# Optimization experiments

Measured on AMD Instinct MI355X. Metric: run time of the kernel, lower is better.

Reference implementation:

```python
import jax, jax.numpy as jnp
import numpy as np

# Sizes: B graphs of N nodes each, K nearest neighbours, D=feat_dim=nhid, C=pos_dim
B, N, K, D, C = 4, 1024, 128, 32, 2
L = 3                     # number of EGNN conv layers
E_IN = 2 * D + 1          # edge MLP input: feats_i | feats_j | rel_dist (edge_dim=0, fourier=0)
E_H = 2 * E_IN            # edge MLP hidden


def _lin(key, fan_in, fan_out):
    kw, kb = jax.random.split(key)
    w = jax.random.normal(kw, (fan_in, fan_out), jnp.float32) / np.sqrt(fan_in)
    b = jax.random.normal(kb, (fan_out,), jnp.float32) * 0.01
    return w, b


def _stack(key, fan_in, fan_out):
    ws, bs = zip(*[_lin(k, fan_in, fan_out) for k in jax.random.split(key, L)])
    return jnp.stack(ws), jnp.stack(bs)


def setup_inputs() -> dict:
    key = jax.random.key(0)
    ks = jax.random.split(key, 10)
    feat_ = jax.random.normal(ks[0], (B * N, D), jnp.float32)
    coor_ = jax.random.normal(ks[1], (B * N, C), jnp.float32)
    batch = jnp.full((B,), N, dtype=jnp.int32)   # per-graph node counts (equal-size graphs)
    embed_w, embed_b = _lin(ks[2], D, D)         # embed: Linear(feat_dim, nhid)
    e1_w, e1_b = _stack(ks[3], E_IN, E_H)        # edge MLP
    e2_w, e2_b = _stack(ks[4], E_H, D)           # -> m_dim = nhid
    gate_w, gate_b = _stack(ks[5], D, 1)         # soft_edges gate
    c1_w, c1_b = _stack(ks[6], D, 4 * D)         # coors MLP
    c2_w, c2_b = _stack(ks[7], 4 * D, 1)
    n1_w, n1_b = _stack(ks[8], 2 * D, 2 * D)     # node MLP
    n2_w, n2_b = _stack(ks[9], 2 * D, D)
    coors_scale = jnp.full((L, 1), 1e-2, jnp.float32)  # CoorsNorm scale (init 1e-2)
    return dict(feat_=feat_, coor_=coor_, batch=batch, embed_w=embed_w, embed_b=embed_b,
                e1_w=e1_w, e1_b=e1_b, e2_w=e2_w, e2_b=e2_b, gate_w=gate_w, gate_b=gate_b,
                c1_w=c1_w, c1_b=c1_b, c2_w=c2_w, c2_b=c2_b, n1_w=n1_w, n1_b=n1_b,
                n2_w=n2_w, n2_b=n2_b, coors_scale=coors_scale)


def _lrelu(x):
    return jax.nn.leaky_relu(x, 0.1)


def _gather(x, idx):
    # x: [B, n, d], idx: [B, n, k] -> [B, n, k, d]
    return jax.vmap(lambda xb, ib: xb[ib])(x, idx)


def _egnn_layer(feats, coors, p):
    (e1_w, e1_b, e2_w, e2_b, gate_w, gate_b, c1_w, c1_b, c2_w, c2_b,
     n1_w, n1_b, n2_w, n2_b, scale) = p
    # pairwise squared distances; k smallest (self included, valid_radius=inf)
    diff = coors[:, :, None, :] - coors[:, None, :, :]      # [B,n,n,C]
    dist = jnp.sum(diff * diff, axis=-1)                    # [B,n,n]
    neg_d, idx = jax.lax.top_k(-dist, K)                    # k nearest
    rel_dist = -neg_d[..., None]                            # [B,n,K,1]
    rel_coors = coors[:, :, None, :] - _gather(coors, idx)  # [B,n,K,C]
    feats_j = _gather(feats, idx)                           # [B,n,K,D]
    feats_i = jnp.broadcast_to(feats[:, :, None, :], feats_j.shape)
    edge_in = jnp.concatenate([feats_i, feats_j, rel_dist], axis=-1)  # [B,n,K,E_IN]
    # edge MLP: Lin -> act -> Lin -> act ; soft edge gate
    m = _lrelu(_lrelu(edge_in @ e1_w + e1_b) @ e2_w + e2_b)            # [B,n,K,D]
    m = m * jax.nn.sigmoid(m @ gate_w + gate_b)
    # coordinate update: coors_mlp -> scalar weights; CoorsNorm on rel coords
    cw = (_lrelu(m @ c1_w + c1_b) @ c2_w + c2_b)[..., 0]               # [B,n,K]
    norm = jnp.maximum(jnp.linalg.norm(rel_coors, axis=-1, keepdims=True), 1e-8)
    rel_n = rel_coors / norm * scale
    coors_out = jnp.einsum('bik,bikc->bic', cw, rel_n) + coors
    # feature update: sum-pool messages, node MLP with residual
    m_i = jnp.sum(m, axis=2)                                           # [B,n,D]
    node_in = jnp.concatenate([feats, m_i], axis=-1)
    feats_out = _lrelu(node_in @ n1_w + n1_b) @ n2_w + n2_b + feats
    return feats_out, coors_out


def reference(feat_, coor_, batch, embed_w, embed_b, e1_w, e1_b, e2_w, e2_b,
              gate_w, gate_b, c1_w, c1_b, c2_w, c2_b, n1_w, n1_b, n2_w, n2_b,
              coors_scale):
    # embed MLP (dropout is identity at p=0 / eval), then batch equal-size graphs
    feats = _lrelu(feat_ @ embed_w + embed_b).reshape(B, N, D)
    coors = coor_.reshape(B, N, C)
    for l in range(L):
        p = (e1_w[l], e1_b[l], e2_w[l], e2_b[l], gate_w[l], gate_b[l],
             c1_w[l], c1_b[l], c2_w[l], c2_b[l], n1_w[l], n1_b[l],
             n2_w[l], n2_b[l], coors_scale[l])
        feats, coors = _egnn_layer(feats, coors, p)
    return feats.reshape(B * N, D)
```

## Files before the change

### kernel.cpp

```cpp
#include <hip/hip_runtime.h>
#include <hip/hip_bf16.h>
#include <math.h>

#define BB 4
#define NN 1024
#define KK 128
#define DD 32
#define LL 3
#define EH 130
#define EHP 132

typedef float f32x4 __attribute__((ext_vector_type(4)));
typedef short s16x8 __attribute__((ext_vector_type(8)));

__device__ __forceinline__ float lrelu(float x) { return fmaxf(x, 0.1f * x); }

__device__ __forceinline__ unsigned pk2(float a, float b) {
    __hip_bfloat162 h = __float22bfloat162_rn(float2{a, b});
    return *(unsigned*)&h;
}
__device__ __forceinline__ unsigned short bf16_hu(float v) {
    return (unsigned short)((__float_as_uint(v) + 0x8000u) >> 16);
}
__device__ __forceinline__ unsigned short bf16_rne(float v) {
    unsigned u = __float_as_uint(v);
    return (unsigned short)((u + 0x7fffu + ((u >> 16) & 1u)) >> 16);
}

__global__ __launch_bounds__(256) void prep_kernel(
    const float* __restrict__ feat, const float* __restrict__ ew, const float* __restrict__ eb,
    float* __restrict__ out,
    const float* __restrict__ e2w, const float* __restrict__ c1w,
    unsigned short* __restrict__ e2f, unsigned short* __restrict__ c1f,
    const float* __restrict__ e1w0, const float* __restrict__ e1b0,
    float* __restrict__ HI, float* __restrict__ HJ) {
    if (blockIdx.x < 512) {
        const int tid = threadIdx.x;
        const int t = blockIdx.x * 256 + tid;
        const int n = t >> 5, o = t & 31;
        __shared__ float sfe[256];
        const float* f = feat + n * DD;
        float a = eb[o];
#pragma unroll
        for (int k = 0; k < DD; k++) a = fmaf(f[k], ew[k * DD + o], a);
        a = lrelu(a);
        out[t] = a;
        sfe[tid] = a;
        __syncthreads();
        for (int idx = tid; idx < 8 * EHP; idx += 256) {
            const int nl = idx / EHP, o2 = idx % EHP;
            const size_t off = (size_t)(blockIdx.x * 8 + nl) * EHP + o2;
            if (o2 >= EH) { HI[off] = 0.f; HJ[off] = 0.f; continue; }
            const float* fl = sfe + nl * DD;
            float aa = e1b0[o2], cc = 0.f;
#pragma unroll
            for (int k = 0; k < DD; k++) aa = fmaf(fl[k], e1w0[k * EH + o2], aa);
#pragma unroll
            for (int k = 0; k < DD; k++) cc = fmaf(fl[k], e1w0[(DD + k) * EH + o2], cc);
            HI[off] = aa;
            HJ[off] = cc;
        }
    } else {
        int t = (blockIdx.x - 512) * 256 + threadIdx.x;
        if (t < LL * 4 * 2 * 512) {
            int jj = t & 7, lane = (t >> 3) & 63, nt = (t >> 9) & 1, c = (t >> 10) & 3, l = t >> 12;
            int k = 32 * c + (lane >> 4) * 8 + jj;
            int n = nt * 16 + (lane & 15);
            e2f[t] = bf16_rne(e2w[(size_t)l * EH * DD + k * DD + n]);
        } else {
            int u = t - LL * 4 * 2 * 512;
            if (u < LL * 8 * 512) {
                int jj = u & 7, lane = (u >> 3) & 63, nt = (u >> 9) & 7, l = u >> 12;
                int k = (lane >> 4) * 8 + jj;
                int n = nt * 16 + (lane & 15);
                c1f[u] = bf16_rne(c1w[(size_t)l * DD * 128 + k * 128 + n]);
            }
        }
    }
}

__global__ __launch_bounds__(128) void layer_kernel(
    const float* __restrict__ feats_in, const float* __restrict__ coors_in,
    const float* __restrict__ HI, const float* __restrict__ HJ,
    float* __restrict__ HIo, float* __restrict__ HJo,
    const float* __restrict__ e1n, const float* __restrict__ e1bn,
    const int donext,
    const float* __restrict__ w65,
    const float* __restrict__ e2w,
    const float* __restrict__ e2b,
    const unsigned short* __restrict__ e2f,
    const unsigned short* __restrict__ c1f,
    const float* __restrict__ gw, const float* __restrict__ gb,
    const float* __restrict__ c1b, const float* __restrict__ c2w, const float* __restrict__ c2b,
    const float* __restrict__ n1w, const float* __restrict__ n1b,
    const float* __restrict__ n2w, const float* __restrict__ n2b,
    const float* __restrict__ scale,
    float* __restrict__ feats_out, float* __restrict__ coors_out) {
    const int node = blockIdx.x;
    const int b = node >> 10, i = node & (NN - 1);
    const int t = threadIdx.x;
    const int lane = t & 63, wid = t >> 6;
    const int ln = lane & 15, q = lane >> 4;
    const int rowbase = wid * 64;

    __shared__ float2 scoor[NN];
    __shared__ int snbr[KK];
    __shared__ __align__(16) float shi[EHP];
    __shared__ __align__(16) float sw65[EHP];
    __shared__ __align__(16) unsigned short smA[2 * 64 * 32];
    __shared__ float sx0[128], sx1[128], su[128], sv[128];
    __shared__ float sgw[DD], se2b[DD], sfi[DD], sfo[DD];
    __shared__ float sc1b[128], sc2w[128];
    __shared__ float redm[2][DD], redc[2][2];
    __shared__ float sni[2 * DD], shd[2 * DD];

    if (wid == 0) {
        const float2* cbp = (const float2*)(coors_in + (size_t)b * NN * 2);
        const float2 ci = cbp[i];
        unsigned k[16];
#pragma unroll
        for (int s = 0; s < 16; s++) {
            float2 cj = cbp[lane + 64 * s];
            scoor[lane + 64 * s] = cj;
            float dx = ci.x - cj.x, dy = ci.y - cj.y;
            float d = __fadd_rn(__fmul_rn(dx, dx), __fmul_rn(dy, dy));
            k[s] = __float_as_uint(d);
        }
        unsigned P = 0;
        for (int bpos = 30; bpos >= 0; bpos--) {
            const unsigned X = P | (1u << bpos);
            unsigned c = 0;
#pragma unroll
            for (int s = 0; s < 16; s++)
                c += (unsigned)__popcll(__ballot(k[s] < X));
            if (c < (unsigned)KK) P = X;
        }
        const unsigned dstar = P;
        const unsigned long long below = (1ull << lane) - 1ull;
        unsigned run = 0;
#pragma unroll
        for (int s = 0; s < 16; s++) {
            unsigned long long m = __ballot(k[s] < dstar);
            if (k[s] < dstar) snbr[run + (unsigned)__popcll(m & below)] = lane + 64 * s;
            run += (unsigned)__popcll(m);
        }
        const int need = KK - (int)run;
        unsigned tie = 0;
        for (int s = 0; s < 16 && (int)tie < need; s++) {
            unsigned long long m = __ballot(k[s] == dstar);
            if (k[s] == dstar) {
                unsigned r = tie + (unsigned)__popcll(m & below);
                if ((int)r < need) snbr[run + r] = lane + 64 * s;
            }
            tie += (unsigned)__popcll(m);
        }
    } else {
        for (int u = lane; u < EHP; u += 64) {
            shi[u] = HI[(size_t)node * EHP + u];
            sw65[u] = (u < EH) ? w65[u] : 0.f;
        }
        if (lane < DD) {
            sfi[lane] = feats_in[node * DD + lane];
            sgw[lane] = gw[lane];
            se2b[lane] = e2b[lane];
        }
        sc1b[lane] = c1b[lane];
        sc1b[lane + 64] = c1b[lane + 64];
        sc2w[lane] = c2w[lane];
        sc2w[lane + 64] = c2w[lane + 64];
    }
    __syncthreads();

    const float2 cif = scoor[i];
    const float cix = cif.x, ciy = cif.y;
    const int j = snbr[t];
    const float2 cj = scoor[j];
    const float dx = cix - cj.x, dy = ciy - cj.y;
    const float rd = __fadd_rn(__fmul_rn(dx, dx), __fmul_rn(dy, dy));
    const float nrm = fmaxf(sqrtf(rd), 1e-8f);
    const float s = scale[0] / nrm;
    su[t] = dx * s;
    sv[t] = dy * s;

    {
        const float2 hjt = *(const float2*)(HJ + ((size_t)(b * NN) + j) * EHP + 128);
        sx0[t] = lrelu(shi[128] + hjt.x + rd * sw65[128]);
        sx1[t] = lrelu(shi[129] + hjt.y + rd * sw65[129]);
    }

    const float* hjb[4];
    float rdR[4];
#pragma unroll
    for (int mt = 0; mt < 4; mt++) {
        int jR = __shfl(j, mt * 16 + ln, 64);
        rdR[mt] = __shfl(rd, mt * 16 + ln, 64);
        hjb[mt] = HJ + ((size_t)(b * NN) + jR) * EHP;
    }

    const float4* shi4 = (const float4*)shi;
    const float4* sw4  = (const float4*)sw65;

    const f32x4 zz = {0.f, 0.f, 0.f, 0.f};
    f32x4 accA[4][2];
#pragma unroll
    for (int mt = 0; mt < 4; mt++) { accA[mt][0] = zz; accA[mt][1] = zz; }

    float4 ha[4], hbv[4];
#pragma unroll
    for (int mt = 0; mt < 4; mt++) {
        const float4* hjp = (const float4*)(hjb[mt] + q * 8);
        ha[mt] = hjp[0];
        hbv[mt] = hjp[1];
    }

#pragma unroll 1
    for (int c = 0; c < 4; c++) {
        s16x8 b0 = *(const s16x8*)(e2f + ((c * 2 + 0) * 64 + lane) * 8);
        s16x8 b1 = *(const s16x8*)(e2f + ((c * 2 + 1) * 64 + lane) * 8);
        float4 nha[4], nhb[4];
        if (c < 3) {
#pragma unroll
            for (int mt = 0; mt < 4; mt++) {
                const float4* hjp = (const float4*)(hjb[mt] + (c + 1) * 32 + q * 8);
                nha[mt] = hjp[0];
                nhb[mt] = hjp[1];
            }
        }
        const int kb = c * 8 + q * 2;
        const float4 hi0 = shi4[kb], hi1 = shi4[kb + 1];
        const float4 wv0 = sw4[kb],  wv1 = sw4[kb + 1];
#pragma unroll
        for (int mt = 0; mt < 4; mt++) {
            const float r = rdR[mt];
            union { s16x8 v; unsigned u[4]; } A;
            A.u[0] = pk2(lrelu(hi0.x + ha[mt].x + r * wv0.x), lrelu(hi0.y + ha[mt].y + r * wv0.y));
            A.u[1] = pk2(lrelu(hi0.z + ha[mt].z + r * wv0.z), lrelu(hi0.w + ha[mt].w + r * wv0.w));
            A.u[2] = pk2(lrelu(hi1.x + hbv[mt].x + r * wv1.x), lrelu(hi1.y + hbv[mt].y + r * wv1.y));
            A.u[3] = pk2(lrelu(hi1.z + hbv[mt].z + r * wv1.z), lrelu(hi1.w + hbv[mt].w + r * wv1.w));
            accA[mt][0] = __builtin_amdgcn_mfma_f32_16x16x32_bf16(A.v, b0, accA[mt][0], 0, 0, 0);
            accA[mt][1] = __builtin_amdgcn_mfma_f32_16x16x32_bf16(A.v, b1, accA[mt][1], 0, 0, 0);
        }
#pragma unroll
        for (int mt = 0; mt < 4; mt++) { ha[mt] = nha[mt]; hbv[mt] = nhb[mt]; }
    }

#pragma unroll
    for (int nt = 0; nt < 2; nt++) {
        const int col = nt * 16 + ln;
        const float w128 = e2w[128 * DD + col];
        const float w129 = e2w[129 * DD + col];
        const float bv = se2b[col];
#pragma unroll
        for (int mt = 0; mt < 4; mt++)
#pragma unroll
            for (int r = 0; r < 4; r++) {
                const int row = rowbase + mt * 16 + q * 4 + r;
                accA[mt][nt][r] = lrelu(accA[mt][nt][r] + bv + sx0[row] * w128 + sx1[row] * w129);
            }
    }

    const float gbv = gb[0];
#pragma unroll
    for (int mt = 0; mt < 4; mt++) {
        float p[4];
#pragma unroll
        for (int r = 0; r < 4; r++)
            p[r] = accA[mt][0][r] * sgw[ln] + accA[mt][1][r] * sgw[16 + ln];
#pragma unroll
        for (int off = 1; off <= 8; off <<= 1)
#pragma unroll
            for (int r = 0; r < 4; r++) p[r] += __shfl_xor(p[r], off);
#pragma unroll
        for (int r = 0; r < 4; r++) {
            const float g = 1.f / (1.f + __expf(-(p[r] + gbv)));
            accA[mt][0][r] *= g;
            accA[mt][1][r] *= g;
        }
    }

    float mi0 = 0.f, mi1 = 0.f;
#pragma unroll
    for (int mt = 0; mt < 4; mt++)
#pragma unroll
        for (int r = 0; r < 4; r++) { mi0 += accA[mt][0][r]; mi1 += accA[mt][1][r]; }
    mi0 += __shfl_xor(mi0, 16); mi0 += __shfl_xor(mi0, 32);
    mi1 += __shfl_xor(mi1, 16); mi1 += __shfl_xor(mi1, 32);
    if (lane < 16) { redm[wid][lane] = mi0; redm[wid][16 + lane] = mi1; }

    unsigned short* smw = smA + wid * (64 * 32);
#pragma unroll
    for (int mt = 0; mt < 4; mt++)
#pragma unroll
        for (int nt = 0; nt < 2; nt++)
#pragma unroll
            for (int r = 0; r < 4; r++) {
                const int prow = (r << 4) | (4 * mt + q);
                smw[prow * 32 + nt * 16 + ln] = bf16_hu(accA[mt][nt][r]);
            }

    s16x8 a4[4];
#pragma unroll
    for (int mt = 0; mt < 4; mt++) {
        const int prow = ((ln & 3) << 4) | (4 * mt + (ln >> 2));
        a4[mt] = *(const s16x8*)(smw + prow * 32 + q * 8);
    }

    float cacc[4][4];
#pragma unroll
    for (int mt = 0; mt < 4; mt++)
#pragma unroll
        for (int r = 0; r < 4; r++) cacc[mt][r] = 0.f;

#pragma unroll 1
    for (int g = 0; g < 4; g++) {
        s16x8 bc0 = *(const s16x8*)(c1f + ((2 * g + 0) * 64 + lane) * 8);
        s16x8 bc1 = *(const s16x8*)(c1f + ((2 * g + 1) * 64 + lane) * 8);
        f32x4 c20[4], c21[4];
#pragma unroll
        for (int mt = 0; mt < 4; mt++) {
            c20[mt] = __builtin_amdgcn_mfma_f32_16x16x32_bf16(a4[mt], bc0, zz, 0, 0, 0);
            c21[mt] = __builtin_amdgcn_mfma_f32_16x16x32_bf16(a4[mt], bc1, zz, 0, 0, 0);
        }
#pragma unroll
        for (int h = 0; h < 2; h++) {
            const int col = (2 * g + h) * 16 + ln;
            const float c1bv = sc1b[col], c2wv = sc2w[col];
#pragma unroll
            for (int mt = 0; mt < 4; mt++)
#pragma unroll
                for (int r = 0; r < 4; r++) {
                    const float v = (h ? c21[mt][r] : c20[mt][r]) + c1bv;
                    cacc[mt][r] = fmaf(lrelu(v), c2wv, cacc[mt][r]);
                }
        }
    }
#pragma unroll
    for (int off = 1; off <= 8; off <<= 1)
#pragma unroll
        for (int mt = 0; mt < 4; mt++)
#pragma unroll
            for (int r = 0; r < 4; r++) cacc[mt][r] += __shfl_xor(cacc[mt][r], off);

    const float c2bv = c2b[0];
    float vxp = 0.f, vyp = 0.f;
    if (ln == 0) {
#pragma unroll
        for (int mt = 0; mt < 4; mt++)
#pragma unroll
            for (int r = 0; r < 4; r++) {
                const int row = rowbase + mt * 16 + q * 4 + r;
                const float cw = cacc[mt][r] + c2bv;
                vxp = fmaf(cw, su[row], vxp);
                vyp = fmaf(cw, sv[row], vyp);
            }
    }
    vxp += __shfl_xor(vxp, 16); vxp += __shfl_xor(vxp, 32);
    vyp += __shfl_xor(vyp, 16); vyp += __shfl_xor(vyp, 32);
    if (lane == 0) { redc[wid][0] = vxp; redc[wid][1] = vyp; }

    __syncthreads();
    if (t < DD) {
        sni[t] = sfi[t];
        sni[DD + t] = redm[0][t] + redm[1][t];
    }
    __syncthreads();
    if (t < 2 * DD) {
        float a = n1b[t];
#pragma unroll
        for (int k = 0; k < 2 * DD; k++) a = fmaf(sni[k], n1w[k * 2 * DD + t], a);
        shd[t] = lrelu(a);
    }
    __syncthreads();
    if (t < DD) {
        float a = n2b[t];
#pragma unroll
        for (int o = 0; o < 2 * DD; o++) a = fmaf(shd[o], n2w[o * DD + t], a);
        const float fo = a + sfi[t];
        feats_out[node * DD + t] = fo;
        sfo[t] = fo;
    }
    if (t == 0) {
        coors_out[node * 2] = cix + redc[0][0] + redc[1][0];
        coors_out[node * 2 + 1] = ciy + redc[0][1] + redc[1][1];
    }
    __syncthreads();

    if (donext) {
        for (int o = t; o < EHP; o += 128) {
            const size_t off = (size_t)node * EHP + o;
            if (o >= EH) { HIo[off] = 0.f; HJo[off] = 0.f; continue; }
            float aa = e1bn[o], cc = 0.f;
#pragma unroll
            for (int k = 0; k < DD; k++) aa = fmaf(sfo[k], e1n[k * EH + o], aa);
#pragma unroll
            for (int k = 0; k < DD; k++) cc = fmaf(sfo[k], e1n[(DD + k) * EH + o], cc);
            HIo[off] = aa;
            HJo[off] = cc;
        }
    }
}

extern "C" void kernel_launch(void* const* d_in, const int* in_sizes, int n_in,
                              void* d_out, int out_size, void* d_ws, size_t ws_size,
                              hipStream_t stream) {
    const float* feat_   = (const float*)d_in[0];
    const float* coor_   = (const float*)d_in[1];
    const float* embed_w = (const float*)d_in[3];
    const float* embed_b = (const float*)d_in[4];
    const float* e1_w    = (const float*)d_in[5];
    const float* e1_b    = (const float*)d_in[6];
    const float* e2_w    = (const float*)d_in[7];
    const float* e2_b    = (const float*)d_in[8];
    const float* gate_w  = (const float*)d_in[9];
    const float* gate_b  = (const float*)d_in[10];
    const float* c1_w    = (const float*)d_in[11];
    const float* c1_b    = (const float*)d_in[12];
    const float* c2_w    = (const float*)d_in[13];
    const float* c2_b    = (const float*)d_in[14];
    const float* n1_w    = (const float*)d_in[15];
    const float* n1_b    = (const float*)d_in[16];
    const float* n2_w    = (const float*)d_in[17];
    const float* n2_b    = (const float*)d_in[18];
    const float* cscale  = (const float*)d_in[19];

    float* ws = (float*)d_ws;
    float* feats_a = ws;               ws += BB * NN * DD;
    float* feats_b = ws;               ws += BB * NN * DD;
    float* coors_a = ws;               ws += BB * NN * 2;
    float* coors_b = ws;               ws += BB * NN * 2;
    float* HI_a    = ws;               ws += BB * NN * EHP;
    float* HJ_a    = ws;               ws += BB * NN * EHP;
    float* HI_b    = ws;               ws += BB * NN * EHP;
    float* HJ_b    = ws;               ws += BB * NN * EHP;
    unsigned short* e2f = (unsigned short*)ws;
    unsigned short* c1f = e2f + LL * 4096;

    prep_kernel<<<512 + 96, 256, 0, stream>>>(feat_, embed_w, embed_b, feats_a,
                                              e2_w, c1_w, e2f, c1f,
                                              e1_w, e1_b, HI_a, HJ_a);

    const float* fin = feats_a;
    const float* cin = coor_;
    float* fouts[LL] = {feats_b, feats_a, (float*)d_out};
    float* couts[LL] = {coors_a, coors_b, coors_a};
    float* HIs[2] = {HI_a, HI_b};
    float* HJs[2] = {HJ_a, HJ_b};

    for (int l = 0; l < LL; l++) {
        const int nl = (l + 1 < LL) ? l + 1 : l;
        layer_kernel<<<BB * NN, 128, 0, stream>>>(
            fin, cin,
            HIs[l & 1], HJs[l & 1],
            HIs[(l + 1) & 1], HJs[(l + 1) & 1],
            e1_w + (size_t)nl * 65 * EH, e1_b + (size_t)nl * EH,
            (l + 1 < LL) ? 1 : 0,
            e1_w + ((size_t)l * 65 + 64) * EH,
            e2_w + (size_t)l * EH * DD,
            e2_b + (size_t)l * DD,
            e2f + (size_t)l * 4096,
            c1f + (size_t)l * 4096,
            gate_w + (size_t)l * DD,
            gate_b + l,
            c1_b + (size_t)l * 128,
            c2_w + (size_t)l * 128,
            c2_b + l,
            n1_w + (size_t)l * 64 * 64,
            n1_b + (size_t)l * 64,
            n2_w + (size_t)l * 64 * 32,
            n2_b + (size_t)l * DD,
            cscale + l,
            fouts[l], couts[l]);
        fin = fouts[l];
        cin = couts[l];
    }
}
```

Before: 381.3 us.

## Split kNN selection out of layer kernel into separate kernel

Moves the per-node radix-select kNN out of the fused layer kernel into its own kernel (folded into the prep kernel for layer 0), writing neighbour indices to global memory. Before, one of two waves in each layer block spent most of its time on the select while the other wave sat idle. The layer kernel now reads neighbour indices and coordinates from global memory and drops the 8KB shared coordinate buffer, which may raise occupancy. This costs extra kernel launches and a global round-trip for the neighbour lists.

```diff
diff --git a/kernel.cpp b/kernel.cpp
--- a/kernel.cpp
+++ b/kernel.cpp
@@ -27,60 +27,119 @@
     return (unsigned short)((u + 0x7fffu + ((u >> 16) & 1u)) >> 16);
 }
 
-__global__ __launch_bounds__(256) void prep_kernel(
-    const float* __restrict__ feat, const float* __restrict__ ew, const float* __restrict__ eb,
-    float* __restrict__ out,
+__device__ __forceinline__ void knn_select(const float2* __restrict__ cbp, int i, int lane,
+                                           int* __restrict__ nb) {
+    const float2 ci = cbp[i];
+    unsigned k[16];
+#pragma unroll
+    for (int s = 0; s < 16; s++) {
+        float2 cj = cbp[lane + 64 * s];
+        float dx = ci.x - cj.x, dy = ci.y - cj.y;
+        float d = __fadd_rn(__fmul_rn(dx, dx), __fmul_rn(dy, dy));
+        k[s] = __float_as_uint(d);
+    }
+    unsigned P = 0;
+    for (int bpos = 30; bpos >= 0; bpos--) {
+        const unsigned X = P | (1u << bpos);
+        unsigned c = 0;
+#pragma unroll
+        for (int s = 0; s < 16; s++)
+            c += (unsigned)__popcll(__ballot(k[s] < X));
+        if (c < (unsigned)KK) P = X;
+    }
+    const unsigned dstar = P;
+    const unsigned long long below = (1ull << lane) - 1ull;
+    unsigned run = 0;
+#pragma unroll
+    for (int s = 0; s < 16; s++) {
+        unsigned long long m = __ballot(k[s] < dstar);
+        if (k[s] < dstar) nb[run + (unsigned)__popcll(m & below)] = lane + 64 * s;
+        run += (unsigned)__popcll(m);
+    }
+    const int need = KK - (int)run;
+    unsigned tie = 0;
+    for (int s = 0; s < 16 && (int)tie < need; s++) {
+        unsigned long long m = __ballot(k[s] == dstar);
+        if (k[s] == dstar) {
+            unsigned r = tie + (unsigned)__popcll(m & below);
+            if ((int)r < need) nb[run + r] = lane + 64 * s;
+        }
+        tie += (unsigned)__popcll(m);
+    }
+}
+
+__global__ __launch_bounds__(128) void prep_kernel(
+    const float* __restrict__ feat, const float* __restrict__ coor,
+    const float* __restrict__ ew, const float* __restrict__ eb,
+    float* __restrict__ fout,
+    const float* __restrict__ e1w0, const float* __restrict__ e1b0,
+    float* __restrict__ HI, float* __restrict__ HJ,
+    int* __restrict__ nbr,
     const float* __restrict__ e2w, const float* __restrict__ c1w,
-    unsigned short* __restrict__ e2f, unsigned short* __restrict__ c1f,
-    const float* __restrict__ e1w0, const float* __restrict__ e1b0,
-    float* __restrict__ HI, float* __restrict__ HJ) {
-    if (blockIdx.x < 512) {
-        const int tid = threadIdx.x;
-        const int t = blockIdx.x * 256 + tid;
-        const int n = t >> 5, o = t & 31;
-        __shared__ float sfe[256];
-        const float* f = feat + n * DD;
-        float a = eb[o];
-#pragma unroll
-        for (int k = 0; k < DD; k++) a = fmaf(f[k], ew[k * DD + o], a);
-        a = lrelu(a);
-        out[t] = a;
-        sfe[tid] = a;
+    unsigned short* __restrict__ e2f, unsigned short* __restrict__ c1f) {
+    const int bid = blockIdx.x;
+    const int t = threadIdx.x;
+    if (bid < 2048) {
+        __shared__ float sfe[2][DD];
+        const int n0 = bid * 2;
+        if (t < 64) {
+            const int nl = t >> 5, o = t & 31;
+            const float* f = feat + (size_t)(n0 + nl) * DD;
+            float a = eb[o];
+#pragma unroll
+            for (int k = 0; k < DD; k++) a = fmaf(f[k], ew[k * DD + o], a);
+            a = lrelu(a);
+            fout[(size_t)(n0 + nl) * DD + o] = a;
+            sfe[nl][o] = a;
+        }
         __syncthreads();
-        for (int idx = tid; idx < 8 * EHP; idx += 256) {
-            const int nl = idx / EHP, o2 = idx % EHP;
-            const size_t off = (size_t)(blockIdx.x * 8 + nl) * EHP + o2;
-            if (o2 >= EH) { HI[off] = 0.f; HJ[off] = 0.f; continue; }
-            const float* fl = sfe + nl * DD;
-            float aa = e1b0[o2], cc = 0.f;
-#pragma unroll
-            for (int k = 0; k < DD; k++) aa = fmaf(fl[k], e1w0[k * EH + o2], aa);
-#pragma unroll
-            for (int k = 0; k < DD; k++) cc = fmaf(fl[k], e1w0[(DD + k) * EH + o2], cc);
+        for (int idx = t; idx < 2 * EHP; idx += 128) {
+            const int nl = idx / EHP, o = idx - nl * EHP;
+            const size_t off = (size_t)(n0 + nl) * EHP + o;
+            if (o >= EH) { HI[off] = 0.f; HJ[off] = 0.f; continue; }
+            const float* fl = sfe[nl];
+            float aa = e1b0[o], cc = 0.f;
+#pragma unroll
+            for (int k = 0; k < DD; k++) aa = fmaf(fl[k], e1w0[k * EH + o], aa);
+#pragma unroll
+            for (int k = 0; k < DD; k++) cc = fmaf(fl[k], e1w0[(DD + k) * EH + o], cc);
             HI[off] = aa;
             HJ[off] = cc;
         }
+    } else if (bid < 4096) {
+        const int node = (bid - 2048) * 2 + (t >> 6);
+        const int b = node >> 10, i = node & (NN - 1);
+        knn_select((const float2*)coor + (size_t)b * NN, i, t & 63,
+                   nbr + (size_t)node * KK);
     } else {
-        int t = (blockIdx.x - 512) * 256 + threadIdx.x;
-        if (t < LL * 4 * 2 * 512) {
-            int jj = t & 7, lane = (t >> 3) & 63, nt = (t >> 9) & 1, c = (t >> 10) & 3, l = t >> 12;
-            int k = 32 * c + (lane >> 4) * 8 + jj;
-            int n = nt * 16 + (lane & 15);
-            e2f[t] = bf16_rne(e2w[(size_t)l * EH * DD + k * DD + n]);
-        } else {
-            int u = t - LL * 4 * 2 * 512;
-            if (u < LL * 8 * 512) {
-                int jj = u & 7, lane = (u >> 3) & 63, nt = (u >> 9) & 7, l = u >> 12;
-                int k = (lane >> 4) * 8 + jj;
-                int n = nt * 16 + (lane & 15);
-                c1f[u] = bf16_rne(c1w[(size_t)l * DD * 128 + k * 128 + n]);
+        for (int u = (bid - 4096) * 128 + t; u < 2 * LL * 4096; u += 96 * 128) {
+            if (u < LL * 4096) {
+                int jj = u & 7, la = (u >> 3) & 63, nt = (u >> 9) & 1, c = (u >> 10) & 3, l = u >> 12;
+                int k = 32 * c + (la >> 4) * 8 + jj;
+                int n = nt * 16 + (la & 15);
+                e2f[u] = bf16_rne(e2w[(size_t)l * EH * DD + k * DD + n]);
+            } else {
+                int v = u - LL * 4096;
+                int jj = v & 7, la = (v >> 3) & 63, nt = (v >> 9) & 7, l = v >> 12;
+                int k = (la >> 4) * 8 + jj;
+                int n = nt * 16 + (la & 15);
+                c1f[v] = bf16_rne(c1w[(size_t)l * DD * 128 + k * 128 + n]);
             }
         }
     }
+}
+
+__global__ __launch_bounds__(256) void knn_kernel(const float* __restrict__ coors,
+                                                  int* __restrict__ nbr) {
+    const int node = (int)blockIdx.x * 4 + (threadIdx.x >> 6);
+    const int b = node >> 10, i = node & (NN - 1);
+    knn_select((const float2*)coors + (size_t)b * NN, i, threadIdx.x & 63,
+               nbr + (size_t)node * KK);
 }
 
 __global__ __launch_bounds__(128) void layer_kernel(
     const float* __restrict__ feats_in, const float* __restrict__ coors_in,
+    const int*   __restrict__ nbr,
     const float* __restrict__ HI, const float* __restrict__ HJ,
     float* __restrict__ HIo, float* __restrict__ HJo,
     const float* __restrict__ e1n, const float* __restrict__ e1bn,
@@ -97,14 +156,12 @@
     const float* __restrict__ scale,
     float* __restrict__ feats_out, float* __restrict__ coors_out) {
     const int node = blockIdx.x;
-    const int b = node >> 10, i = node & (NN - 1);
+    const int b = node >> 10;
     const int t = threadIdx.x;
     const int lane = t & 63, wid = t >> 6;
     const int ln = lane & 15, q = lane >> 4;
     const int rowbase = wid * 64;
 
-    __shared__ float2 scoor[NN];
-    __shared__ int snbr[KK];
     __shared__ __align__(16) float shi[EHP];
     __shared__ __align__(16) float sw65[EHP];
     __shared__ __align__(16) unsigned short smA[2 * 64 * 32];
@@ -114,67 +171,18 @@
     __shared__ float redm[2][DD], redc[2][2];
     __shared__ float sni[2 * DD], shd[2 * DD];
 
-    if (wid == 0) {
-        const float2* cbp = (const float2*)(coors_in + (size_t)b * NN * 2);
-        const float2 ci = cbp[i];
-        unsigned k[16];
-#pragma unroll
-        for (int s = 0; s < 16; s++) {
-            float2 cj = cbp[lane + 64 * s];
-            scoor[lane + 64 * s] = cj;
-            float dx = ci.x - cj.x, dy = ci.y - cj.y;
-            float d = __fadd_rn(__fmul_rn(dx, dx), __fmul_rn(dy, dy));
-            k[s] = __float_as_uint(d);
-        }
-        unsigned P = 0;
-        for (int bpos = 30; bpos >= 0; bpos--) {
-            const unsigned X = P | (1u << bpos);
-            unsigned c = 0;
-#pragma unroll
-            for (int s = 0; s < 16; s++)
-                c += (unsigned)__popcll(__ballot(k[s] < X));
-            if (c < (unsigned)KK) P = X;
-        }
-        const unsigned dstar = P;
-        const unsigned long long below = (1ull << lane) - 1ull;
-        unsigned run = 0;
-#pragma unroll
-        for (int s = 0; s < 16; s++) {
-            unsigned long long m = __ballot(k[s] < dstar);
-            if (k[s] < dstar) snbr[run + (unsigned)__popcll(m & below)] = lane + 64 * s;
-            run += (unsigned)__popcll(m);
-        }
-        const int need = KK - (int)run;
-        unsigned tie = 0;
-        for (int s = 0; s < 16 && (int)tie < need; s++) {
-            unsigned long long m = __ballot(k[s] == dstar);
-            if (k[s] == dstar) {
-                unsigned r = tie + (unsigned)__popcll(m & below);
-                if ((int)r < need) snbr[run + r] = lane + 64 * s;
-            }
-            tie += (unsigned)__popcll(m);
-        }
-    } else {
-        for (int u = lane; u < EHP; u += 64) {
-            shi[u] = HI[(size_t)node * EHP + u];
-            sw65[u] = (u < EH) ? w65[u] : 0.f;
-        }
-        if (lane < DD) {
-            sfi[lane] = feats_in[node * DD + lane];
-            sgw[lane] = gw[lane];
-            se2b[lane] = e2b[lane];
-        }
-        sc1b[lane] = c1b[lane];
-        sc1b[lane + 64] = c1b[lane + 64];
-        sc2w[lane] = c2w[lane];
-        sc2w[lane + 64] = c2w[lane + 64];
-    }
+    for (int u = t; u < EHP; u += 128) {
+        shi[u] = HI[(size_t)node * EHP + u];
+        sw65[u] = (u < EH) ? w65[u] : 0.f;
+    }
+    if (t < DD) { sfi[t] = feats_in[node * DD + t]; sgw[t] = gw[t]; se2b[t] = e2b[t]; }
+    sc1b[t] = c1b[t];
+    sc2w[t] = c2w[t];
     __syncthreads();
 
-    const float2 cif = scoor[i];
-    const float cix = cif.x, ciy = cif.y;
-    const int j = snbr[t];
-    const float2 cj = scoor[j];
+    const float cix = coors_in[node * 2], ciy = coors_in[node * 2 + 1];
+    const int j = nbr[(size_t)node * KK + t];
+    const float2 cj = *(const float2*)(coors_in + ((size_t)(b * NN) + j) * 2);
     const float dx = cix - cj.x, dy = ciy - cj.y;
     const float rd = __fadd_rn(__fmul_rn(dx, dx), __fmul_rn(dy, dy));
     const float nrm = fmaxf(sqrtf(rd), 1e-8f);
@@ -424,32 +432,35 @@
     const float* cscale  = (const float*)d_in[19];
 
     float* ws = (float*)d_ws;
-    float* feats_a = ws;               ws += BB * NN * DD;
-    float* feats_b = ws;               ws += BB * NN * DD;
-    float* coors_a = ws;               ws += BB * NN * 2;
-    float* coors_b = ws;               ws += BB * NN * 2;
-    float* HI_a    = ws;               ws += BB * NN * EHP;
-    float* HJ_a    = ws;               ws += BB * NN * EHP;
-    float* HI_b    = ws;               ws += BB * NN * EHP;
-    float* HJ_b    = ws;               ws += BB * NN * EHP;
+    float* fa   = ws;   ws += BB * NN * DD;
+    float* fb   = ws;   ws += BB * NN * DD;
+    float* ca   = ws;   ws += BB * NN * 2;
+    float* cb2  = ws;   ws += BB * NN * 2;
+    float* HIa  = ws;   ws += BB * NN * EHP;
+    float* HJa  = ws;   ws += BB * NN * EHP;
+    float* HIb  = ws;   ws += BB * NN * EHP;
+    float* HJb  = ws;   ws += BB * NN * EHP;
     unsigned short* e2f = (unsigned short*)ws;
     unsigned short* c1f = e2f + LL * 4096;
-
-    prep_kernel<<<512 + 96, 256, 0, stream>>>(feat_, embed_w, embed_b, feats_a,
-                                              e2_w, c1_w, e2f, c1f,
-                                              e1_w, e1_b, HI_a, HJ_a);
-
-    const float* fin = feats_a;
+    int* nbr = (int*)(c1f + LL * 4096);
+
+    prep_kernel<<<4096 + 96, 128, 0, stream>>>(feat_, coor_, embed_w, embed_b, fa,
+                                               e1_w, e1_b, HIa, HJa, nbr,
+                                               e2_w, c1_w, e2f, c1f);
+
+    const float* fin = fa;
     const float* cin = coor_;
-    float* fouts[LL] = {feats_b, feats_a, (float*)d_out};
-    float* couts[LL] = {coors_a, coors_b, coors_a};
-    float* HIs[2] = {HI_a, HI_b};
-    float* HJs[2] = {HJ_a, HJ_b};
+    float* fouts[LL] = {fb, fa, (float*)d_out};
+    float* couts[LL] = {ca, cb2, ca};
+    float* HIs[2] = {HIa, HIb};
+    float* HJs[2] = {HJa, HJb};
 
     for (int l = 0; l < LL; l++) {
+        if (l > 0)
+            knn_kernel<<<BB * NN / 4, 256, 0, stream>>>(cin, nbr);
         const int nl = (l + 1 < LL) ? l + 1 : l;
         layer_kernel<<<BB * NN, 128, 0, stream>>>(
-            fin, cin,
+            fin, cin, nbr,
             HIs[l & 1], HJs[l & 1],
             HIs[(l + 1) & 1], HJs[(l + 1) & 1],
             e1_w + (size_t)nl * 65 * EH, e1_b + (size_t)nl * EH,
```

Measured after the change: 345.1 us. -9.5%, faster.
